# Performance work log

Hardware: AMD Instinct MI355X
Metric: run time of the kernel (lower is better)

The kernel has to match this reference:

```python
import jax, jax.numpy as jnp
import numpy as np

S, B, D, H = 2048, 2, 1024, 16
DH = D // H
WINDOW = 256
DILATION = 1


def setup_inputs() -> dict:
    key = jax.random.key(0)
    ks = jax.random.split(key, 10)
    scale = 1.0 / np.sqrt(D)
    x = jax.random.normal(ks[0], (S, B, D), dtype=jnp.float32)
    Wq = jax.random.normal(ks[1], (D, D), dtype=jnp.float32) * scale
    Wk = jax.random.normal(ks[2], (D, D), dtype=jnp.float32) * scale
    Wv = jax.random.normal(ks[3], (D, D), dtype=jnp.float32) * scale
    Wo = jax.random.normal(ks[4], (D, D), dtype=jnp.float32) * scale
    bq = jax.random.normal(ks[5], (D,), dtype=jnp.float32) * 0.01
    bk = jax.random.normal(ks[6], (D,), dtype=jnp.float32) * 0.01
    bv = jax.random.normal(ks[7], (D,), dtype=jnp.float32) * 0.01
    bo = jax.random.normal(ks[8], (D,), dtype=jnp.float32) * 0.01
    beta = jax.random.normal(ks[9], (H,), dtype=jnp.float32) * 0.1
    return {"x": x, "Wq": Wq, "bq": bq, "Wk": Wk, "bk": bk,
            "Wv": Wv, "bv": bv, "Wo": Wo, "bo": bo, "beta": beta}


def _causal_window_bias(seq_len, window_len, dilation):
    # allowed iff 0 <= i-j <= dilation*(window_len-1) and (i-j) % dilation == 0
    idx = jnp.arange(seq_len)
    diff = idx[:, None] - idx[None, :]
    allowed = (diff >= 0) & (diff <= dilation * (window_len - 1)) & (diff % dilation == 0)
    return jnp.where(allowed, 0.0, -jnp.inf).astype(jnp.float32)  # [S, S]


def reference(x, Wq, bq, Wk, bk, Wv, bv, Wo, bo, beta):
    s, b, d = x.shape
    # projections (torch Linear: x @ W.T + b)
    q = x @ Wq.T + bq
    k = x @ Wk.T + bk
    v = x @ Wv.T + bv
    # 's b (h d) -> b h s d'
    q = q.reshape(s, b, H, DH).transpose(1, 2, 0, 3)
    k = k.reshape(s, b, H, DH).transpose(1, 2, 0, 3)
    v = v.reshape(s, b, H, DH).transpose(1, 2, 0, 3)
    # per-head beta scaling: q / (sqrt(d_head) * exp(beta))
    q = q / (np.sqrt(DH) * jnp.exp(beta)[None, :, None, None])
    bias = _causal_window_bias(s, WINDOW, DILATION)  # [S, S]
    scores = jnp.einsum('bhqd,bhkd->bhqk', q, k) + bias[None, None]
    p = jax.nn.softmax(scores, axis=-1)
    out = jnp.einsum('bhqk,bhkd->bhqd', p, v)
    # 'b h s d -> s b (h d)'
    out = out.transpose(2, 0, 1, 3).reshape(s, b, d)
    return out @ Wo.T + bo
```

## Files before the change

### kernel.cpp

```cpp
#include <hip/hip_runtime.h>
#include <hip/hip_bf16.h>

#define S_LEN 2048
#define BATCH 2
#define DMODEL 1024
#define NHEAD 16
#define DHEAD 64
#define WINDOW 256
#define MROWS (S_LEN * BATCH)

typedef unsigned short u16;
typedef unsigned int u32;
typedef __attribute__((ext_vector_type(8))) short bf16x8;
typedef __attribute__((ext_vector_type(4))) float f32x4;
typedef __attribute__((ext_vector_type(2))) unsigned int u32x2;

typedef const __attribute__((address_space(1))) void gvoid;
typedef __attribute__((address_space(3))) void lvoid;

__device__ __forceinline__ float b2f(u16 u) {
    union { unsigned int i; float f; } x; x.i = ((unsigned int)u) << 16; return x.f;
}
__device__ __forceinline__ u16 f2b(float f) {
    union { float f; unsigned int i; } x; x.f = f;
    unsigned int r = x.i + 0x7fffu + ((x.i >> 16) & 1u);
    return (u16)(r >> 16);
}
__device__ __forceinline__ u32 cvtpk(float a, float b) {
    u32 r; asm("v_cvt_pk_bf16_f32 %0, %1, %2" : "=v"(r) : "v"(a), "v"(b)); return r;
}
__device__ __forceinline__ bf16x8 ld8f(const float* __restrict__ p) {
    bf16x8 r;
    #pragma unroll
    for (int i = 0; i < 8; i++) r[i] = (short)f2b(p[i]);
    return r;
}
template<bool BF>
__device__ __forceinline__ bf16x8 ldrow(const void* __restrict__ base, size_t elemOff) {
    if constexpr (BF) return *reinterpret_cast<const bf16x8*>((const u16*)base + elemOff);
    else              return ld8f((const float*)base + elemOff);
}

__global__ __launch_bounds__(256) void cast_all(
    const float* __restrict__ x,  const float* __restrict__ Wq,
    const float* __restrict__ Wk, const float* __restrict__ Wv,
    const float* __restrict__ Wo,
    u16* __restrict__ xb, u16* __restrict__ wb, u16* __restrict__ wob)
{
    const size_t idx = ((size_t)blockIdx.x * 256 + threadIdx.x) * 8;
    const size_t M1 = 1048576;
    const float* src; u16* dst;
    if (idx < 4 * M1)      { src = x  + idx;            dst = xb  + idx; }
    else if (idx < 5 * M1) { src = Wq + (idx - 4 * M1); dst = wb  + (idx - 4 * M1); }
    else if (idx < 6 * M1) { src = Wk + (idx - 5 * M1); dst = wb  + (idx - 4 * M1); }
    else if (idx < 7 * M1) { src = Wv + (idx - 6 * M1); dst = wb  + (idx - 4 * M1); }
    else                   { src = Wo + (idx - 7 * M1); dst = wob + (idx - 7 * M1); }
    *reinterpret_cast<bf16x8*>(dst) = ld8f(src);
}

__global__ __launch_bounds__(256) void gemm_qkv_s(
    const u16* __restrict__ A, const u16* __restrict__ Wall,
    const float* __restrict__ bq, const float* __restrict__ bk, const float* __restrict__ bv,
    const float* __restrict__ beta,
    u16* __restrict__ qbuf, u16* __restrict__ kbuf, u16* __restrict__ vt)
{
    __shared__ u16 lA[128 * 32];
    __shared__ u16 lB[128 * 32];
    const int tid = threadIdx.x;
    const int lane = tid & 63, wave = tid >> 6;
    const int r15 = lane & 15, g = lane >> 4;
    const int m0 = blockIdx.x * 128;
    const int range = blockIdx.y >> 3;
    const int n0 = (blockIdx.y & 7) * 128;
    const u16* W = Wall + (size_t)range * DMODEL * DMODEL;
    const float* bias = (range == 0) ? bq : (range == 1) ? bk : bv;

    const int srow = tid >> 2;
    const int sslot = (tid & 3) ^ ((tid >> 3) & 3);
    const u16* aSrc = A + (size_t)(m0 + srow) * DMODEL + sslot * 8;
    const u16* wSrc = W + (size_t)(n0 + srow) * DMODEL + sslot * 8;
    const int ldsW = wave * 1024;
    const int mrow = (wave >> 1) * 64, nrow = (wave & 1) * 64;
    const int swz = (g ^ ((r15 >> 1) & 3)) << 4;
    const char* lAr = (const char*)lA + swz;
    const char* lBr = (const char*)lB + swz;

    f32x4 acc[4][4] = {};
    for (int kk = 0; kk < DMODEL; kk += 32) {
        __syncthreads();
        #pragma unroll
        for (int ro = 0; ro < 2; ro++) {
            __builtin_amdgcn_global_load_lds(
                (gvoid*)(aSrc + (size_t)ro * 64 * DMODEL + kk),
                (lvoid*)((char*)lA + ro * 4096 + ldsW), 16, 0, 0);
            __builtin_amdgcn_global_load_lds(
                (gvoid*)(wSrc + (size_t)ro * 64 * DMODEL + kk),
                (lvoid*)((char*)lB + ro * 4096 + ldsW), 16, 0, 0);
        }
        __syncthreads();
        bf16x8 af[4], bf[4];
        #pragma unroll
        for (int mi = 0; mi < 4; mi++)
            af[mi] = *reinterpret_cast<const bf16x8*>(lAr + ((mrow + mi * 16 + r15) << 6));
        #pragma unroll
        for (int ni = 0; ni < 4; ni++)
            bf[ni] = *reinterpret_cast<const bf16x8*>(lBr + ((nrow + ni * 16 + r15) << 6));
        #pragma unroll
        for (int mi = 0; mi < 4; mi++)
            #pragma unroll
            for (int ni = 0; ni < 4; ni++)
                acc[mi][ni] = __builtin_amdgcn_mfma_f32_16x16x32_bf16(
                    af[mi], bf[ni], acc[mi][ni], 0, 0, 0);
    }
    #pragma unroll
    for (int ni = 0; ni < 4; ni++) {
        const int col = n0 + nrow + ni * 16 + r15;
        const float bv_ = bias[col];
        float scale = 1.0f;
        if (range == 0) scale = 1.0f / (8.0f * __expf(beta[col >> 6]));
        #pragma unroll
        for (int mi = 0; mi < 4; mi++)
            #pragma unroll
            for (int r = 0; r < 4; r++) {
                const int row = m0 + mrow + mi * 16 + g * 4 + r;
                const float val = acc[mi][ni][r] + bv_;
                if (range == 0) {
                    qbuf[(size_t)row * DMODEL + col] = f2b(val * scale);
                } else if (range == 1) {
                    kbuf[(size_t)row * DMODEL + col] = f2b(val);
                } else {
                    const int b = row & 1, s = row >> 1;
                    vt[((size_t)(b * NHEAD + (col >> 6)) * DHEAD + (col & 63)) * S_LEN + s]
                        = f2b(val);
                }
            }
    }
}

__global__ __launch_bounds__(256) void gemm_out_s(
    const u16* __restrict__ A, const u16* __restrict__ W,
    const float* __restrict__ bias, float* __restrict__ C)
{
    __shared__ u16 lA[128 * 32];
    __shared__ u16 lB[128 * 32];
    const int tid = threadIdx.x;
    const int lane = tid & 63, wave = tid >> 6;
    const int r15 = lane & 15, g = lane >> 4;
    const int m0 = blockIdx.x * 128;
    const int n0 = blockIdx.y * 128;

    const int srow = tid >> 2;
    const int sslot = (tid & 3) ^ ((tid >> 3) & 3);
    const u16* aSrc = A + (size_t)(m0 + srow) * DMODEL + sslot * 8;
    const u16* wSrc = W + (size_t)(n0 + srow) * DMODEL + sslot * 8;
    const int ldsW = wave * 1024;
    const int mrow = (wave >> 1) * 64, nrow = (wave & 1) * 64;
    const int swz = (g ^ ((r15 >> 1) & 3)) << 4;
    const char* lAr = (const char*)lA + swz;
    const char* lBr = (const char*)lB + swz;

    f32x4 acc[4][4] = {};
    for (int kk = 0; kk < DMODEL; kk += 32) {
        __syncthreads();
        #pragma unroll
        for (int ro = 0; ro < 2; ro++) {
            __builtin_amdgcn_global_load_lds(
                (gvoid*)(aSrc + (size_t)ro * 64 * DMODEL + kk),
                (lvoid*)((char*)lA + ro * 4096 + ldsW), 16, 0, 0);
            __builtin_amdgcn_global_load_lds(
                (gvoid*)(wSrc + (size_t)ro * 64 * DMODEL + kk),
                (lvoid*)((char*)lB + ro * 4096 + ldsW), 16, 0, 0);
        }
        __syncthreads();
        bf16x8 af[4], bf[4];
        #pragma unroll
        for (int mi = 0; mi < 4; mi++)
            af[mi] = *reinterpret_cast<const bf16x8*>(lAr + ((mrow + mi * 16 + r15) << 6));
        #pragma unroll
        for (int ni = 0; ni < 4; ni++)
            bf[ni] = *reinterpret_cast<const bf16x8*>(lBr + ((nrow + ni * 16 + r15) << 6));
        #pragma unroll
        for (int mi = 0; mi < 4; mi++)
            #pragma unroll
            for (int ni = 0; ni < 4; ni++)
                acc[mi][ni] = __builtin_amdgcn_mfma_f32_16x16x32_bf16(
                    af[mi], bf[ni], acc[mi][ni], 0, 0, 0);
    }
    #pragma unroll
    for (int ni = 0; ni < 4; ni++) {
        const int col = n0 + nrow + ni * 16 + r15;
        const float bv_ = bias[col];
        #pragma unroll
        for (int mi = 0; mi < 4; mi++)
            #pragma unroll
            for (int r = 0; r < 4; r++) {
                const int row = m0 + mrow + mi * 16 + g * 4 + r;
                C[(size_t)row * DMODEL + col] = acc[mi][ni][r] + bv_;
            }
    }
}

template<bool ABF, bool WBF>
__global__ __launch_bounds__(256) void gemm_qkv_t(
    const void* __restrict__ A_,
    const void* __restrict__ Wq_, const void* __restrict__ Wk_, const void* __restrict__ Wv_,
    const float* __restrict__ bq, const float* __restrict__ bk, const float* __restrict__ bv,
    const float* __restrict__ beta,
    u16* __restrict__ qbuf, u16* __restrict__ kbuf, u16* __restrict__ vt)
{
    const int lane = threadIdx.x & 63;
    const int wave = threadIdx.x >> 6;
    const int r15 = lane & 15, g = lane >> 4;
    const int m0 = blockIdx.x * 128 + (wave >> 1) * 64;
    const int range = blockIdx.y >> 3;
    const int n0 = (blockIdx.y & 7) * 128 + (wave & 1) * 64;
    const void* W_ = (range == 0) ? Wq_ : (range == 1) ? Wk_ : Wv_;
    const float* bias = (range == 0) ? bq : (range == 1) ? bk : bv;
    const size_t aBase = (size_t)(m0 + r15) * DMODEL + g * 8;
    const size_t wBase = (size_t)(n0 + r15) * DMODEL + g * 8;
    f32x4 acc[4][4] = {};
    for (int k = 0; k < DMODEL; k += 32) {
        bf16x8 af[4], bf[4];
        #pragma unroll
        for (int mi = 0; mi < 4; mi++) af[mi] = ldrow<ABF>(A_, aBase + (size_t)mi * 16 * DMODEL + k);
        #pragma unroll
        for (int ni = 0; ni < 4; ni++) bf[ni] = ldrow<WBF>(W_, wBase + (size_t)ni * 16 * DMODEL + k);
        #pragma unroll
        for (int mi = 0; mi < 4; mi++)
            #pragma unroll
            for (int ni = 0; ni < 4; ni++)
                acc[mi][ni] = __builtin_amdgcn_mfma_f32_16x16x32_bf16(
                    af[mi], bf[ni], acc[mi][ni], 0, 0, 0);
    }
    #pragma unroll
    for (int ni = 0; ni < 4; ni++) {
        const int col = n0 + ni * 16 + r15;
        const float bv_ = bias[col];
        float scale = 1.0f;
        if (range == 0) scale = 1.0f / (8.0f * __expf(beta[col >> 6]));
        #pragma unroll
        for (int mi = 0; mi < 4; mi++)
            #pragma unroll
            for (int r = 0; r < 4; r++) {
                const int row = m0 + mi * 16 + g * 4 + r;
                const float val = acc[mi][ni][r] + bv_;
                if (range == 0) {
                    qbuf[(size_t)row * DMODEL + col] = f2b(val * scale);
                } else if (range == 1) {
                    kbuf[(size_t)row * DMODEL + col] = f2b(val);
                } else {
                    const int b = row & 1, s = row >> 1;
                    vt[((size_t)(b * NHEAD + (col >> 6)) * DHEAD + (col & 63)) * S_LEN + s]
                        = f2b(val);
                }
            }
    }
}

template<bool WBF>
__global__ __launch_bounds__(256) void gemm_out_t(
    const u16* __restrict__ A, const void* __restrict__ W_,
    const float* __restrict__ bias, float* __restrict__ C)
{
    const int lane = threadIdx.x & 63;
    const int wave = threadIdx.x >> 6;
    const int r15 = lane & 15, g = lane >> 4;
    const int m0 = blockIdx.x * 64 + (wave >> 1) * 32;
    const int n0 = blockIdx.y * 128 + (wave & 1) * 64;
    const u16* a0 = A + (size_t)(m0 + r15) * DMODEL + g * 8;
    const size_t wBase = (size_t)(n0 + r15) * DMODEL + g * 8;
    f32x4 acc[2][4] = {};
    for (int k = 0; k < DMODEL; k += 32) {
        bf16x8 af[2], bf[4];
        #pragma unroll
        for (int mi = 0; mi < 2; mi++)
            af[mi] = *reinterpret_cast<const bf16x8*>(a0 + (size_t)mi * 16 * DMODEL + k);
        #pragma unroll
        for (int ni = 0; ni < 4; ni++) bf[ni] = ldrow<WBF>(W_, wBase + (size_t)ni * 16 * DMODEL + k);
        #pragma unroll
        for (int mi = 0; mi < 2; mi++)
            #pragma unroll
            for (int ni = 0; ni < 4; ni++)
                acc[mi][ni] = __builtin_amdgcn_mfma_f32_16x16x32_bf16(
                    af[mi], bf[ni], acc[mi][ni], 0, 0, 0);
    }
    #pragma unroll
    for (int ni = 0; ni < 4; ni++) {
        const int col = n0 + ni * 16 + r15;
        const float bv_ = bias[col];
        #pragma unroll
        for (int mi = 0; mi < 2; mi++)
            #pragma unroll
            for (int r = 0; r < 4; r++) {
                const int row = m0 + mi * 16 + g * 4 + r;
                C[(size_t)row * DMODEL + col] = acc[mi][ni][r] + bv_;
            }
    }
}

__global__ __launch_bounds__(256) void attn6(
    const u16* __restrict__ qb, const u16* __restrict__ kb_,
    const u16* __restrict__ vt, u16* __restrict__ O)
{
    __shared__ u16 lK[64 * 64];
    __shared__ u16 lV[64 * 64];
    __shared__ u16 plds[4][16][64];
    const int tid  = threadIdx.x;
    const int lane = tid & 63;
    const int wave = tid >> 6;
    const int bid  = blockIdx.x;
    const int sbid = (bid & 7) * 128 + (bid >> 3);
    const int qblk = sbid & 31;
    const int h    = (sbid >> 5) & (NHEAD - 1);
    const int b    = sbid >> 9;
    const int qt = qblk * 4 + wave;
    const int qstart = qt * 16;
    const int r15 = lane & 15, g = lane >> 4;
    const int i_glob = qstart + r15;

    const u16* qrow = qb + ((size_t)i_glob * BATCH + b) * DMODEL + h * DHEAD;
    const bf16x8 qf0 = *reinterpret_cast<const bf16x8*>(qrow + g * 8);
    const bf16x8 qf1 = *reinterpret_cast<const bf16x8*>(qrow + 32 + g * 8);

    char* prow = (char*)plds + wave * 2048 + r15 * 128;
    const int q7 = r15 & 7;

    const int sr_lo = wave * 8 + (lane >> 3);
    const int scol8 = lane & 7;

    float psum = 0.0f;
    f32x4 o[4] = {};

    #pragma unroll
    for (int c = 0; c < 5; c++) {
        const int kstart = qblk * 64 - WINDOW + c * 64;
        if (kstart < -63) continue;

        __syncthreads();
        #pragma unroll
        for (int i = 0; i < 2; i++) {
            const int srow = i * 32 + sr_lo;
            const int sc = scol8 ^ (srow & 7);
            const int ks = min(max(kstart + srow, 0), S_LEN - 1);
            __builtin_amdgcn_global_load_lds(
                (gvoid*)(kb_ + ((size_t)ks * BATCH + b) * DMODEL + h * DHEAD + sc * 8),
                (lvoid*)((char*)lK + i * 4096 + wave * 1024), 16, 0, 0);
            const int vs = min(max(kstart + sc * 8, 0), S_LEN - 8);
            __builtin_amdgcn_global_load_lds(
                (gvoid*)(vt + ((size_t)(b * NHEAD + h) * DHEAD + srow) * S_LEN + vs),
                (lvoid*)((char*)lV + i * 4096 + wave * 1024), 16, 0, 0);
        }
        __syncthreads();

        f32x4 st[4] = {};
        #pragma unroll
        for (int t = 0; t < 4; t++) {
            const int R = t * 16 + r15;
            const bf16x8 ka = *reinterpret_cast<const bf16x8*>(
                lK + R * 64 + ((g ^ (R & 7)) << 3));
            const bf16x8 kc = *reinterpret_cast<const bf16x8*>(
                lK + R * 64 + (((4 + g) ^ (R & 7)) << 3));
            st[t] = __builtin_amdgcn_mfma_f32_16x16x32_bf16(ka, qf0, st[t], 0, 0, 0);
            st[t] = __builtin_amdgcn_mfma_f32_16x16x32_bf16(kc, qf1, st[t], 0, 0, 0);
        }

        #pragma unroll
        for (int t = 0; t < 4; t++) {
            float p[4];
            #pragma unroll
            for (int r = 0; r < 4; r++) {
                const int j = kstart + t * 16 + g * 4 + r;
                const int d = i_glob - j;
                p[r] = (j < 0 || d < 0 || d >= WINDOW) ? 0.0f : __expf(st[t][r]);
                psum += p[r];
            }
            u32x2 w;
            w.x = cvtpk(p[0], p[1]);
            w.y = cvtpk(p[2], p[3]);
            *reinterpret_cast<u32x2*>(
                prow + ((((t << 1) + (g >> 1)) ^ q7) << 4) + ((g & 1) << 3)) = w;
        }
        const bf16x8 pf0 = *reinterpret_cast<const bf16x8*>(prow + ((g ^ q7) << 4));
        const bf16x8 pf1 = *reinterpret_cast<const bf16x8*>(prow + (((4 + g) ^ q7) << 4));

        #pragma unroll
        for (int c4 = 0; c4 < 4; c4++) {
            const int R = c4 * 16 + r15;
            const bf16x8 vf0 = *reinterpret_cast<const bf16x8*>(
                lV + R * 64 + ((g ^ (R & 7)) << 3));
            const bf16x8 vf1 = *reinterpret_cast<const bf16x8*>(
                lV + R * 64 + (((4 + g) ^ (R & 7)) << 3));
            o[c4] = __builtin_amdgcn_mfma_f32_16x16x32_bf16(vf0, pf0, o[c4], 0, 0, 0);
            o[c4] = __builtin_amdgcn_mfma_f32_16x16x32_bf16(vf1, pf1, o[c4], 0, 0, 0);
        }
    }

    psum += __shfl_xor(psum, 16);
    psum += __shfl_xor(psum, 32);
    const float inv = 1.0f / psum;
    #pragma unroll
    for (int c4 = 0; c4 < 4; c4++)
        #pragma unroll
        for (int r = 0; r < 4; r++) {
            const int dh = c4 * 16 + g * 4 + r;
            O[((size_t)i_glob * BATCH + b) * DMODEL + h * DHEAD + dh] = f2b(o[c4][r] * inv);
        }
}

extern "C" void kernel_launch(void* const* d_in, const int* in_sizes, int n_in,
                              void* d_out, int out_size, void* d_ws, size_t ws_size,
                              hipStream_t stream) {
    const float* x    = (const float*)d_in[0];
    const float* Wq   = (const float*)d_in[1];
    const float* bq   = (const float*)d_in[2];
    const float* Wk   = (const float*)d_in[3];
    const float* bk   = (const float*)d_in[4];
    const float* Wv   = (const float*)d_in[5];
    const float* bv   = (const float*)d_in[6];
    const float* Wo   = (const float*)d_in[7];
    const float* bo   = (const float*)d_in[8];
    const float* beta = (const float*)d_in[9];
    float* out = (float*)d_out;
    u16* ws = (u16*)d_ws;

    const size_t M4 = (size_t)MROWS * DMODEL;
    u16* qbuf = (u16*)d_out;
    u16* kbuf = (u16*)d_out + M4;
    u16* vtb  = ws;
    u16* abuf = ws + M4;

    const int nattn = BATCH * NHEAD * (S_LEN / 64);
    dim3 gqkv(MROWS / 128, 24);
    dim3 gout(MROWS / 128, 8);

    if (ws_size >= (size_t)32 * 1024 * 1024) {
        u16* xb  = ws + 2 * M4;
        u16* wb  = ws + 3 * M4;
        u16* wob = ws + 3 * M4 + 3145728;
        cast_all<<<4096, 256, 0, stream>>>(x, Wq, Wk, Wv, Wo, xb, wb, wob);
        gemm_qkv_s<<<gqkv, 256, 0, stream>>>(xb, wb, bq, bk, bv, beta, qbuf, kbuf, vtb);
        attn6<<<nattn, 256, 0, stream>>>(qbuf, kbuf, vtb, abuf);
        gemm_out_s<<<gout, 256, 0, stream>>>(abuf, wob, bo, out);
    } else {
        dim3 gout2(MROWS / 64, 8);
        gemm_qkv_t<false, false><<<gqkv, 256, 0, stream>>>(
            x, Wq, Wk, Wv, bq, bk, bv, beta, qbuf, kbuf, vtb);
        attn6<<<nattn, 256, 0, stream>>>(qbuf, kbuf, vtb, abuf);
        gemm_out_t<false><<<gout2, 256, 0, stream>>>(abuf, Wo, bo, out);
    }
}
```

Measured before the change: 93.08 us.

## Rewrite QKV GEMM as 256x256-tile, 8-wave double-buffered pipelined kernel

The QKV projection GEMM moves from 128x128 tiles with 4 waves and single-buffered K=32 steps to 256x256 tiles with 8 waves, K=64 steps and double-buffered LDS. Global-to-LDS loads for the next K slice are issued in two halves interleaved with the MFMA work, and explicit waitcnt, barriers and setprio are used to overlap memory traffic with compute. This is meant to raise data reuse per tile and hide load latency. The grid shrinks to 16x12 = 192 blocks, which may underfill the CUs, and the larger LDS footprint and register use limit occupancy.

```diff
diff --git a/kernel.cpp b/kernel.cpp
--- a/kernel.cpp
+++ b/kernel.cpp
@@ -58,71 +58,126 @@
     *reinterpret_cast<bf16x8*>(dst) = ld8f(src);
 }
 
-__global__ __launch_bounds__(256) void gemm_qkv_s(
+__global__ __launch_bounds__(512, 2) void gemm_qkv_8p(
     const u16* __restrict__ A, const u16* __restrict__ Wall,
     const float* __restrict__ bq, const float* __restrict__ bk, const float* __restrict__ bv,
     const float* __restrict__ beta,
     u16* __restrict__ qbuf, u16* __restrict__ kbuf, u16* __restrict__ vt)
 {
-    __shared__ u16 lA[128 * 32];
-    __shared__ u16 lB[128 * 32];
+    __shared__ u16 sA[2][2][128 * 64];
+    __shared__ u16 sB[2][2][128 * 64];
     const int tid = threadIdx.x;
     const int lane = tid & 63, wave = tid >> 6;
     const int r15 = lane & 15, g = lane >> 4;
-    const int m0 = blockIdx.x * 128;
-    const int range = blockIdx.y >> 3;
-    const int n0 = (blockIdx.y & 7) * 128;
+    const int wm = wave >> 2, wn = wave & 3;
+    const int m0 = blockIdx.x * 256;
+    const int range = blockIdx.y >> 2;
+    const int n0 = (blockIdx.y & 3) * 256;
     const u16* W = Wall + (size_t)range * DMODEL * DMODEL;
     const float* bias = (range == 0) ? bq : (range == 1) ? bk : bv;
 
-    const int srow = tid >> 2;
-    const int sslot = (tid & 3) ^ ((tid >> 3) & 3);
-    const u16* aSrc = A + (size_t)(m0 + srow) * DMODEL + sslot * 8;
-    const u16* wSrc = W + (size_t)(n0 + srow) * DMODEL + sslot * 8;
-    const int ldsW = wave * 1024;
-    const int mrow = (wave >> 1) * 64, nrow = (wave & 1) * 64;
-    const int swz = (g ^ ((r15 >> 1) & 3)) << 4;
-    const char* lAr = (const char*)lA + swz;
-    const char* lBr = (const char*)lB + swz;
-
-    f32x4 acc[4][4] = {};
-    for (int kk = 0; kk < DMODEL; kk += 32) {
-        __syncthreads();
-        #pragma unroll
-        for (int ro = 0; ro < 2; ro++) {
-            __builtin_amdgcn_global_load_lds(
-                (gvoid*)(aSrc + (size_t)ro * 64 * DMODEL + kk),
-                (lvoid*)((char*)lA + ro * 4096 + ldsW), 16, 0, 0);
-            __builtin_amdgcn_global_load_lds(
-                (gvoid*)(wSrc + (size_t)ro * 64 * DMODEL + kk),
-                (lvoid*)((char*)lB + ro * 4096 + ldsW), 16, 0, 0);
-        }
-        __syncthreads();
-        bf16x8 af[4], bf[4];
-        #pragma unroll
-        for (int mi = 0; mi < 4; mi++)
-            af[mi] = *reinterpret_cast<const bf16x8*>(lAr + ((mrow + mi * 16 + r15) << 6));
+    const int srow = tid >> 3;
+    const int sls  = (tid & 7) ^ (srow & 7);
+    const u16* aS = A + (size_t)(m0 + srow) * DMODEL + sls * 8;
+    const u16* wS = W + (size_t)(n0 + srow) * DMODEL + sls * 8;
+
+    auto stgA = [&](int bufi, int h, int rb, int koff) {
+        __builtin_amdgcn_global_load_lds(
+            (gvoid*)(aS + (size_t)(h * 128 + rb * 64) * DMODEL + koff),
+            (lvoid*)((char*)&sA[bufi][h][0] + rb * 8192 + wave * 1024), 16, 0, 0);
+    };
+    auto stgB = [&](int bufi, int h, int rb, int koff) {
+        __builtin_amdgcn_global_load_lds(
+            (gvoid*)(wS + (size_t)(h * 128 + rb * 64) * DMODEL + koff),
+            (lvoid*)((char*)&sB[bufi][h][0] + rb * 8192 + wave * 1024), 16, 0, 0);
+    };
+    const int pswz = r15 & 7;
+    auto ldA = [&](int bufi, int mi, int ks) {
+        return *reinterpret_cast<const bf16x8*>(
+            (const char*)&sA[bufi][wm][0] + ((mi * 16 + r15) << 7)
+            + (((ks * 4 + g) ^ pswz) << 4));
+    };
+    auto ldB = [&](int bufi, int ni, int ks) {
+        return *reinterpret_cast<const bf16x8*>(
+            (const char*)&sB[bufi][wn >> 1][0] + (((wn & 1) * 64 + ni * 16 + r15) << 7)
+            + (((ks * 4 + g) ^ pswz) << 4));
+    };
+
+    stgB(0, 0, 0, 0); stgB(0, 1, 0, 0); stgB(0, 0, 1, 0); stgB(0, 1, 1, 0);
+    stgA(0, 0, 1, 0); stgA(0, 1, 1, 0); stgA(0, 0, 0, 0); stgA(0, 1, 0, 0);
+    asm volatile("s_waitcnt vmcnt(0)" ::: "memory");
+    __builtin_amdgcn_sched_barrier(0);
+    __builtin_amdgcn_s_barrier();
+    __builtin_amdgcn_sched_barrier(0);
+
+    f32x4 acc[8][4] = {};
+    for (int j = 0; j < 16; ++j) {
+        const int buf = j & 1, nbuf = buf ^ 1;
+        const int koff = (j + 1) * 64;
+        bf16x8 bfr[4][2];
+        if (j < 15) {
+            stgB(nbuf, 0, 0, koff); stgB(nbuf, 1, 0, koff);
+            stgB(nbuf, 0, 1, koff); stgB(nbuf, 1, 1, koff);
+            __builtin_amdgcn_sched_barrier(0);
+            asm volatile("s_waitcnt vmcnt(4)" ::: "memory");
+        } else {
+            asm volatile("s_waitcnt vmcnt(0)" ::: "memory");
+        }
+        __builtin_amdgcn_sched_barrier(0);
+        __builtin_amdgcn_s_barrier();
+        __builtin_amdgcn_sched_barrier(0);
         #pragma unroll
         for (int ni = 0; ni < 4; ni++)
-            bf[ni] = *reinterpret_cast<const bf16x8*>(lBr + ((nrow + ni * 16 + r15) << 6));
-        #pragma unroll
-        for (int mi = 0; mi < 4; mi++)
-            #pragma unroll
-            for (int ni = 0; ni < 4; ni++)
-                acc[mi][ni] = __builtin_amdgcn_mfma_f32_16x16x32_bf16(
-                    af[mi], bf[ni], acc[mi][ni], 0, 0, 0);
-    }
+            #pragma unroll
+            for (int ks = 0; ks < 2; ks++) bfr[ni][ks] = ldB(buf, ni, ks);
+        __builtin_amdgcn_s_setprio(1);
+        #pragma unroll
+        for (int mi = 0; mi < 4; mi++) {
+            const bf16x8 a0 = ldA(buf, mi, 0), a1 = ldA(buf, mi, 1);
+            #pragma unroll
+            for (int ni = 0; ni < 4; ni++) {
+                acc[mi][ni] = __builtin_amdgcn_mfma_f32_16x16x32_bf16(
+                    a0, bfr[ni][0], acc[mi][ni], 0, 0, 0);
+                acc[mi][ni] = __builtin_amdgcn_mfma_f32_16x16x32_bf16(
+                    a1, bfr[ni][1], acc[mi][ni], 0, 0, 0);
+            }
+        }
+        __builtin_amdgcn_s_setprio(0);
+        __builtin_amdgcn_sched_barrier(0);
+        if (j < 15) {
+            stgA(nbuf, 0, 1, koff); stgA(nbuf, 1, 1, koff);
+            stgA(nbuf, 0, 0, koff); stgA(nbuf, 1, 0, koff);
+        }
+        __builtin_amdgcn_sched_barrier(0);
+        __builtin_amdgcn_s_barrier();
+        __builtin_amdgcn_sched_barrier(0);
+        __builtin_amdgcn_s_setprio(1);
+        #pragma unroll
+        for (int mi = 4; mi < 8; mi++) {
+            const bf16x8 a0 = ldA(buf, mi, 0), a1 = ldA(buf, mi, 1);
+            #pragma unroll
+            for (int ni = 0; ni < 4; ni++) {
+                acc[mi][ni] = __builtin_amdgcn_mfma_f32_16x16x32_bf16(
+                    a0, bfr[ni][0], acc[mi][ni], 0, 0, 0);
+                acc[mi][ni] = __builtin_amdgcn_mfma_f32_16x16x32_bf16(
+                    a1, bfr[ni][1], acc[mi][ni], 0, 0, 0);
+            }
+        }
+        __builtin_amdgcn_s_setprio(0);
+        __builtin_amdgcn_sched_barrier(0);
+    }
+
     #pragma unroll
     for (int ni = 0; ni < 4; ni++) {
-        const int col = n0 + nrow + ni * 16 + r15;
+        const int col = n0 + wn * 64 + ni * 16 + r15;
         const float bv_ = bias[col];
         float scale = 1.0f;
         if (range == 0) scale = 1.0f / (8.0f * __expf(beta[col >> 6]));
         #pragma unroll
-        for (int mi = 0; mi < 4; mi++)
+        for (int mi = 0; mi < 8; mi++)
             #pragma unroll
             for (int r = 0; r < 4; r++) {
-                const int row = m0 + mrow + mi * 16 + g * 4 + r;
+                const int row = m0 + wm * 128 + mi * 16 + g * 4 + r;
                 const float val = acc[mi][ni][r] + bv_;
                 if (range == 0) {
                     qbuf[(size_t)row * DMODEL + col] = f2b(val * scale);
@@ -430,7 +485,6 @@
     u16* abuf = ws + M4;
 
     const int nattn = BATCH * NHEAD * (S_LEN / 64);
-    dim3 gqkv(MROWS / 128, 24);
     dim3 gout(MROWS / 128, 8);
 
     if (ws_size >= (size_t)32 * 1024 * 1024) {
@@ -438,10 +492,12 @@
         u16* wb  = ws + 3 * M4;
         u16* wob = ws + 3 * M4 + 3145728;
         cast_all<<<4096, 256, 0, stream>>>(x, Wq, Wk, Wv, Wo, xb, wb, wob);
-        gemm_qkv_s<<<gqkv, 256, 0, stream>>>(xb, wb, bq, bk, bv, beta, qbuf, kbuf, vtb);
+        dim3 g8(MROWS / 256, 12);
+        gemm_qkv_8p<<<g8, 512, 0, stream>>>(xb, wb, bq, bk, bv, beta, qbuf, kbuf, vtb);
         attn6<<<nattn, 256, 0, stream>>>(qbuf, kbuf, vtb, abuf);
         gemm_out_s<<<gout, 256, 0, stream>>>(abuf, wob, bo, out);
     } else {
+        dim3 gqkv(MROWS / 128, 24);
         dim3 gout2(MROWS / 64, 8);
         gemm_qkv_t<false, false><<<gqkv, 256, 0, stream>>>(
             x, Wq, Wk, Wv, bq, bk, bv, beta, qbuf, kbuf, vtb);
```

New measurement: 112.2 us. 1.21x slower.
